# Optimization experiments

Measured on AMD Instinct MI355X. Metric: run time of the kernel, lower is better.

Reference implementation:

```python
import jax, jax.numpy as jnp
import numpy as np

N_DRUG = 10000
N_DIS = 10000
FM = 256
FD = 256
E = 320000
LAYERS = 5
OC = 128


def setup_inputs() -> dict:
    key = jax.random.key(0)
    ks = jax.random.split(key, 24)
    s = 1.0 / np.sqrt(FM)  # keep 5 stacked relu-GCN layers numerically tame
    return {
        "x_m": jax.random.normal(ks[0], (N_DRUG, FM), jnp.float32),
        "x_d": jax.random.normal(ks[1], (N_DIS, FD), jnp.float32),
        "w_m": jax.random.uniform(ks[2], (E,), jnp.float32),
        "w_d": jax.random.uniform(ks[3], (E,), jnp.float32),
        "Wx": jax.random.normal(ks[4], (LAYERS, FM, FM), jnp.float32) * s,
        "bx": jnp.zeros((LAYERS, FM), jnp.float32),
        "Wy": jax.random.normal(ks[5], (LAYERS, FD, FD), jnp.float32) * s,
        "by": jnp.zeros((LAYERS, FD), jnp.float32),
        "fc1x_w": jax.random.normal(ks[6], (5 * LAYERS, LAYERS), jnp.float32) * 0.3,
        "fc1x_b": jnp.zeros((5 * LAYERS,), jnp.float32),
        "fc2x_w": jax.random.normal(ks[7], (LAYERS, 5 * LAYERS), jnp.float32) * 0.2,
        "fc2x_b": jnp.zeros((LAYERS,), jnp.float32),
        "fc1y_w": jax.random.normal(ks[8], (5 * LAYERS, LAYERS), jnp.float32) * 0.3,
        "fc1y_b": jnp.zeros((5 * LAYERS,), jnp.float32),
        "fc2y_w": jax.random.normal(ks[9], (LAYERS, 5 * LAYERS), jnp.float32) * 0.2,
        "fc2y_b": jnp.zeros((LAYERS,), jnp.float32),
        "cnnx_w": jax.random.normal(ks[10], (OC, LAYERS, FM, 1), jnp.float32) * 0.05,
        "cnnx_b": jnp.zeros((OC,), jnp.float32),
        "cnny_w": jax.random.normal(ks[11], (OC, LAYERS, FD, 1), jnp.float32) * 0.05,
        "cnny_b": jnp.zeros((OC,), jnp.float32),
        "edges_m": jax.random.randint(ks[12], (2, E), 0, N_DRUG, jnp.int32),
        "edges_d": jax.random.randint(ks[13], (2, E), 0, N_DIS, jnp.int32),
    }


def _gcn_layer(x, W, b, src, dst, ew, n):
    """PyG GCNConv: add self-loops (weight 1), symmetric normalization,
    weighted scatter-add aggregation, then bias."""
    loops = jnp.arange(n)
    src2 = jnp.concatenate([src, loops])
    dst2 = jnp.concatenate([dst, loops])
    w2 = jnp.concatenate([ew, jnp.ones((n,), x.dtype)])
    deg = jax.ops.segment_sum(w2, dst2, num_segments=n)
    dinv = jnp.where(deg > 0, jax.lax.rsqrt(deg), 0.0)
    norm = dinv[src2] * w2 * dinv[dst2]          # [E+n]
    h = x @ W                                     # [n, f]
    agg = jax.ops.segment_sum(norm[:, None] * h[src2], dst2, num_segments=n)
    return agg + b


def _branch(x0, W, b, src, dst, ew, fc1w, fc1b, fc2w, fc2b, cw, cb):
    n = x0.shape[0]
    feats = []
    h = x0
    for i in range(LAYERS):
        h = jax.nn.relu(_gcn_layer(h, W[i], b[i], src, dst, ew, n))
        feats.append(h.T)                          # [f, n]
    X = jnp.stack(feats)                           # [C=5, f, n]  (== XM.view)
    att = jnp.max(X, axis=(1, 2))                  # global max pool -> [5]
    att = jax.nn.relu(att @ fc1w.T + fc1b)
    att = jax.nn.sigmoid(att @ fc2w.T + fc2b)      # [5]
    Xa = jax.nn.relu(att[:, None, None] * X)       # channel attention
    # conv with kernel (f,1): out[o,n] = sum_{c,f} cw[o,c,f,0] * Xa[c,f,n]
    out = jnp.einsum('ocf,cfn->on', cw[..., 0], Xa) + cb[:, None]
    return out.T                                   # [n, out_channels]


def reference(x_m, x_d, w_m, w_d, Wx, bx, Wy, by,
              fc1x_w, fc1x_b, fc2x_w, fc2x_b,
              fc1y_w, fc1y_b, fc2y_w, fc2y_b,
              cnnx_w, cnnx_b, cnny_w, cnny_b,
              edges_m, edges_d):
    x = _branch(x_m, Wx, bx, edges_m[0], edges_m[1], w_m,
                fc1x_w, fc1x_b, fc2x_w, fc2x_b, cnnx_w, cnnx_b)
    y = _branch(x_d, Wy, by, edges_d[0], edges_d[1], w_d,
                fc1y_w, fc1y_b, fc2y_w, fc2y_b, cnny_w, cnny_b)
    return x @ y.T                                 # [N_drug, N_disease]
```

## Files before the change

kernel.cpp:

```cpp
#include <hip/hip_runtime.h>
#include <hip/hip_bf16.h>
#include <math.h>

#define N_NODES 10000
#define FEAT    256
#define NEDGE   320000
#define NLAYERS 5
#define NOC     128

#define NTILE   79
#define PADROWS 10112
#define PACKSZ  1294336

typedef __attribute__((ext_vector_type(8))) short bf16x8;
typedef __attribute__((ext_vector_type(4))) float f32x4;

__global__ void k_init(float* deg, int* cnt, int* fill, int* attm) {
    int i = blockIdx.x * blockDim.x + threadIdx.x;
    if (i < N_NODES) { deg[i] = 1.0f; cnt[i] = 0; fill[i] = 0; }
    if (i < NLAYERS) attm[i] = 0;
}

__global__ void k_count(const int* __restrict__ edges, const float* __restrict__ ew,
                        float* deg, int* cnt) {
    int e = blockIdx.x * blockDim.x + threadIdx.x;
    if (e >= NEDGE) return;
    int d = edges[NEDGE + e];
    atomicAdd(&deg[d], ew[e]);
    atomicAdd(&cnt[d], 1);
}

__global__ void k_dinv(float* deg) {
    int i = blockIdx.x * blockDim.x + threadIdx.x;
    if (i < N_NODES) {
        float dg = deg[i];
        deg[i] = (dg > 0.f) ? 1.0f / sqrtf(dg) : 0.f;
    }
}

__global__ void k_scan(const int* __restrict__ cnt, int* __restrict__ ptr) {
    __shared__ int sm[1024];
    __shared__ int carry;
    int t = threadIdx.x;
    if (t == 0) carry = 0;
    __syncthreads();
    for (int base = 0; base < N_NODES; base += 1024) {
        int i = base + t;
        int v = (i < N_NODES) ? cnt[i] : 0;
        sm[t] = v;
        __syncthreads();
        for (int off = 1; off < 1024; off <<= 1) {
            int add = (t >= off) ? sm[t - off] : 0;
            __syncthreads();
            sm[t] += add;
            __syncthreads();
        }
        if (i < N_NODES) ptr[i] = carry + sm[t] - v;
        __syncthreads();
        if (t == 1023) carry += sm[1023];
        __syncthreads();
    }
    if (t == 0) ptr[N_NODES] = carry;
}

__global__ void k_fill(const int* __restrict__ edges, const float* __restrict__ ew,
                       const float* __restrict__ dinv, const int* __restrict__ ptr,
                       int* fill, int* __restrict__ col, float* __restrict__ val) {
    int e = blockIdx.x * blockDim.x + threadIdx.x;
    if (e >= NEDGE) return;
    int s = edges[e], d = edges[NEDGE + e];
    int pos = ptr[d] + atomicAdd(&fill[d], 1);
    col[pos] = s;
    val[pos] = dinv[s] * ew[e] * dinv[d];
}

__global__ __launch_bounds__(256) void k_spmm(const float* __restrict__ x,
        const int* __restrict__ ptr, const int* __restrict__ col,
        const float* __restrict__ val, const float* __restrict__ dinv,
        float* __restrict__ t) {
    int wave = threadIdx.x >> 6;
    int lane = threadIdx.x & 63;
    int row = blockIdx.x * 4 + wave;
    if (row >= N_NODES) return;
    float di = dinv[row];
    float selfc = di * di;
    float4 xv = ((const float4*)(x + (size_t)row * FEAT))[lane];
    float4 acc;
    acc.x = selfc * xv.x; acc.y = selfc * xv.y; acc.z = selfc * xv.z; acc.w = selfc * xv.w;
    int e0 = ptr[row], e1 = ptr[row + 1];
    for (int e = e0; e < e1; ++e) {
        int c = col[e];
        float cv = val[e];
        float4 v = ((const float4*)(x + (size_t)c * FEAT))[lane];
        acc.x += cv * v.x; acc.y += cv * v.y; acc.z += cv * v.z; acc.w += cv * v.w;
    }
    ((float4*)(t + (size_t)row * FEAT))[lane] = acc;
}

__global__ __launch_bounds__(256) void k_gemm(const float* __restrict__ A,
        const float* __restrict__ B, const float* __restrict__ bias,
        float* __restrict__ C, int M, int N, int K, int chunked,
        int* attm, int do_relu) {
    __shared__ float As[16][68];
    __shared__ float Bs[16][68];
    int tid = threadIdx.x;
    int tx = tid & 15, ty = tid >> 4;
    int m0 = blockIdx.x * 64, n0 = blockIdx.y * 64;
    float acc[4][4];
#pragma unroll
    for (int i = 0; i < 4; ++i)
#pragma unroll
        for (int j = 0; j < 4; ++j) acc[i][j] = 0.f;

    int arow = m0 + (tid >> 2); if (arow >= M) arow = M - 1;
    int am = tid >> 2;
    int akk = (tid & 3) * 4;
    int bk = tid >> 4;
    int bn = (tid & 15) * 4;

    for (int k0 = 0; k0 < K; k0 += 16) {
        int ka = k0 + akk;
        float4 av;
        if (chunked)
            av = *(const float4*)(A + ((size_t)(ka >> 8) * N_NODES + arow) * FEAT + (ka & 255));
        else
            av = *(const float4*)(A + (size_t)arow * K + ka);
        float4 bv = *(const float4*)(B + (size_t)(k0 + bk) * N + (n0 + bn));
        __syncthreads();
        As[akk + 0][am] = av.x;
        As[akk + 1][am] = av.y;
        As[akk + 2][am] = av.z;
        As[akk + 3][am] = av.w;
        *(float4*)&Bs[bk][bn] = bv;
        __syncthreads();
#pragma unroll
        for (int kk = 0; kk < 16; ++kk) {
            float4 a4 = *(const float4*)&As[kk][ty * 4];
            float4 b4 = *(const float4*)&Bs[kk][tx * 4];
            float a[4] = {a4.x, a4.y, a4.z, a4.w};
            float b[4] = {b4.x, b4.y, b4.z, b4.w};
#pragma unroll
            for (int i = 0; i < 4; ++i)
#pragma unroll
                for (int j = 0; j < 4; ++j) acc[i][j] += a[i] * b[j];
        }
    }

    float lmax = 0.f;
#pragma unroll
    for (int i = 0; i < 4; ++i) {
        int m = m0 + ty * 4 + i;
        if (m < M) {
            float vals[4];
#pragma unroll
            for (int j = 0; j < 4; ++j) {
                float v = acc[i][j] + bias[n0 + tx * 4 + j];
                if (do_relu) { v = fmaxf(v, 0.f); lmax = fmaxf(lmax, v); }
                vals[j] = v;
            }
            *(float4*)(C + (size_t)m * N + n0 + tx * 4) =
                make_float4(vals[0], vals[1], vals[2], vals[3]);
        }
    }
    if (do_relu) {
        __syncthreads();
        float* red = (float*)As;
        red[tid] = lmax;
        __syncthreads();
        for (int s = 128; s > 0; s >>= 1) {
            if (tid < s) red[tid] = fmaxf(red[tid], red[tid + s]);
            __syncthreads();
        }
        if (tid == 0) atomicMax(attm, __float_as_int(red[0]));
    }
}

__global__ void k_att(const int* __restrict__ attm, const float* __restrict__ fc1w,
                      const float* __restrict__ fc1b, const float* __restrict__ fc2w,
                      const float* __restrict__ fc2b, float* __restrict__ att) {
    __shared__ float a0[NLAYERS], a1[5 * NLAYERS];
    int t = threadIdx.x;
    if (t < NLAYERS) a0[t] = __int_as_float(attm[t]);
    __syncthreads();
    if (t < 5 * NLAYERS) {
        float s = fc1b[t];
        for (int c = 0; c < NLAYERS; ++c) s += fc1w[t * NLAYERS + c] * a0[c];
        a1[t] = fmaxf(s, 0.f);
    }
    __syncthreads();
    if (t < NLAYERS) {
        float s = fc2b[t];
        for (int c = 0; c < 5 * NLAYERS; ++c) s += fc2w[t * 5 * NLAYERS + c] * a1[c];
        att[t] = 1.f / (1.f + expf(-s));
    }
}

__global__ void k_bprime(const float* __restrict__ cw, const float* __restrict__ att,
                         float* __restrict__ bp) {
    int idx = blockIdx.x * blockDim.x + threadIdx.x;
    if (idx >= NLAYERS * FEAT * NOC) return;
    int k = idx >> 7;
    int o = idx & (NOC - 1);
    bp[idx] = cw[(size_t)o * (NLAYERS * FEAT) + k] * att[k >> 8];
}

__global__ __launch_bounds__(256) void k_pack(const float* __restrict__ src,
        ushort* __restrict__ hi, ushort* __restrict__ lo) {
    int t = blockIdx.x * blockDim.x + threadIdx.x;
    int row = t >> 4;
    int g = t & 15;
    int mt = row >> 4, rr = row & 15;
    int ks = g >> 2, kg = g & 3;
    size_t dst = ((size_t)(mt * 4 + ks) * 64 + kg * 16 + rr) * 8;
    uint h[4] = {0, 0, 0, 0}, l[4] = {0, 0, 0, 0};
    if (row < N_NODES) {
        const float* p = src + (size_t)row * NOC + g * 8;
#pragma unroll
        for (int e = 0; e < 8; ++e) {
            float x = p[e];
            __hip_bfloat16 hb = __float2bfloat16(x);
            float hf = __bfloat162float(hb);
            __hip_bfloat16 lb = __float2bfloat16(x - hf);
            uint hu = *(const ushort*)&hb;
            uint lu = *(const ushort*)&lb;
            h[e >> 1] |= hu << ((e & 1) * 16);
            l[e >> 1] |= lu << ((e & 1) * 16);
        }
    }
    *(uint4*)(hi + dst) = make_uint4(h[0], h[1], h[2], h[3]);
    *(uint4*)(lo + dst) = make_uint4(l[0], l[1], l[2], l[3]);
}

__global__ __launch_bounds__(256) void k_final_mfma(
        const ushort* __restrict__ xh, const ushort* __restrict__ xl,
        const ushort* __restrict__ yh, const ushort* __restrict__ yl,
        float* __restrict__ C) {
    int bid = blockIdx.x;
    const int nwg = NTILE * NTILE;
    const int q = nwg >> 3, r = nwg & 7;
    int xcd = bid & 7, loc = bid >> 3;
    int wg = (xcd < r ? xcd * (q + 1) : r * (q + 1) + (xcd - r) * q) + loc;
    int tm = wg / NTILE, tn = wg % NTILE;

    int tid = threadIdx.x;
    int wave = tid >> 6, lane = tid & 63;
    int m0 = tm * 128 + (wave >> 1) * 64;
    int n0 = tn * 128 + (wave & 1) * 64;
    int mtb = m0 >> 4, ntb = n0 >> 4;

    f32x4 acc[4][4];
#pragma unroll
    for (int i = 0; i < 4; ++i)
#pragma unroll
        for (int j = 0; j < 4; ++j) acc[i][j] = (f32x4){0.f, 0.f, 0.f, 0.f};

#pragma unroll
    for (int ks = 0; ks < 4; ++ks) {
        bf16x8 ah[4], al[4], bh[4], bl[4];
#pragma unroll
        for (int i = 0; i < 4; ++i) {
            size_t ao = ((size_t)((mtb + i) * 4 + ks) * 64 + lane) * 8;
            size_t bo = ((size_t)((ntb + i) * 4 + ks) * 64 + lane) * 8;
            ah[i] = *(const bf16x8*)(xh + ao);
            al[i] = *(const bf16x8*)(xl + ao);
            bh[i] = *(const bf16x8*)(yh + bo);
            bl[i] = *(const bf16x8*)(yl + bo);
        }
#pragma unroll
        for (int i = 0; i < 4; ++i)
#pragma unroll
            for (int j = 0; j < 4; ++j) {
                acc[i][j] = __builtin_amdgcn_mfma_f32_16x16x32_bf16(ah[i], bh[j], acc[i][j], 0, 0, 0);
                acc[i][j] = __builtin_amdgcn_mfma_f32_16x16x32_bf16(ah[i], bl[j], acc[i][j], 0, 0, 0);
                acc[i][j] = __builtin_amdgcn_mfma_f32_16x16x32_bf16(al[i], bh[j], acc[i][j], 0, 0, 0);
            }
    }

    int rbase = (lane >> 4) * 4, cn = lane & 15;
    bool full = (m0 + 63 < N_NODES) && (n0 + 63 < N_NODES);
    if (full) {
#pragma unroll
        for (int i = 0; i < 4; ++i)
#pragma unroll
            for (int j = 0; j < 4; ++j) {
                size_t base = (size_t)(m0 + i * 16 + rbase) * N_NODES + (n0 + j * 16 + cn);
#pragma unroll
                for (int rr = 0; rr < 4; ++rr)
                    C[base + (size_t)rr * N_NODES] = acc[i][j][rr];
            }
    } else {
        for (int i = 0; i < 4; ++i)
            for (int j = 0; j < 4; ++j) {
                int ccol = n0 + j * 16 + cn;
                if (ccol >= N_NODES) continue;
                for (int rr = 0; rr < 4; ++rr) {
                    int mr = m0 + i * 16 + rbase + rr;
                    if (mr < N_NODES)
                        C[(size_t)mr * N_NODES + ccol] = acc[i][j][rr];
                }
            }
    }
}

extern "C" void kernel_launch(void* const* d_in, const int* in_sizes, int n_in,
                              void* d_out, int out_size, void* d_ws, size_t ws_size,
                              hipStream_t stream) {
    (void)in_sizes; (void)n_in; (void)out_size; (void)ws_size;

    float* ws     = (float*)d_ws;
    float* feats  = ws;
    float* tbuf   = feats + 12800000;
    float* outx   = tbuf + 2560000;
    float* outy   = outx + 1280000;
    float* dinv   = outy + 1280000;
    float* val    = dinv + 10016;
    float* bprime = val + 320000;
    float* attF   = bprime + 163840;
    int*   ptr    = (int*)(attF + 16);
    int*   cnt    = ptr + 10016;
    int*   fill   = cnt + 10016;
    int*   col    = fill + 10016;
    int*   attm   = col + 320000;

    ushort* pxh = (ushort*)feats;
    ushort* pxl = pxh + PACKSZ;
    ushort* pyh = pxl + PACKSZ;
    ushort* pyl = pyh + PACKSZ;

    for (int b = 0; b < 2; ++b) {
        const float* x0   = (const float*)d_in[b == 0 ? 0 : 1];
        const float* ew   = (const float*)d_in[b == 0 ? 2 : 3];
        const float* W    = (const float*)d_in[b == 0 ? 4 : 6];
        const float* bias = (const float*)d_in[b == 0 ? 5 : 7];
        const float* fc1w = (const float*)d_in[b == 0 ? 8 : 12];
        const float* fc1b = (const float*)d_in[b == 0 ? 9 : 13];
        const float* fc2w = (const float*)d_in[b == 0 ? 10 : 14];
        const float* fc2b = (const float*)d_in[b == 0 ? 11 : 15];
        const float* cw   = (const float*)d_in[b == 0 ? 16 : 18];
        const float* cb   = (const float*)d_in[b == 0 ? 17 : 19];
        const int* edges  = (const int*)d_in[b == 0 ? 20 : 21];
        float* outb = (b == 0) ? outx : outy;

        k_init<<<40, 256, 0, stream>>>(dinv, cnt, fill, attm);
        k_count<<<1250, 256, 0, stream>>>(edges, ew, dinv, cnt);
        k_dinv<<<40, 256, 0, stream>>>(dinv);
        k_scan<<<1, 1024, 0, stream>>>(cnt, ptr);
        k_fill<<<1250, 256, 0, stream>>>(edges, ew, dinv, ptr, fill, col, val);

        for (int l = 0; l < NLAYERS; ++l) {
            const float* prev = (l == 0) ? x0 : (feats + (size_t)(l - 1) * N_NODES * FEAT);
            k_spmm<<<2500, 256, 0, stream>>>(prev, ptr, col, val, dinv, tbuf);
            k_gemm<<<dim3(157, 4), 256, 0, stream>>>(
                tbuf, W + (size_t)l * FEAT * FEAT, bias + (size_t)l * FEAT,
                feats + (size_t)l * N_NODES * FEAT,
                N_NODES, FEAT, FEAT, 0, attm + l, 1);
        }

        k_att<<<1, 64, 0, stream>>>(attm, fc1w, fc1b, fc2w, fc2b, attF);
        k_bprime<<<640, 256, 0, stream>>>(cw, attF, bprime);
        k_gemm<<<dim3(157, 2), 256, 0, stream>>>(
            feats, bprime, cb, outb, N_NODES, NOC, NLAYERS * FEAT, 1, nullptr, 0);
    }

    k_pack<<<632, 256, 0, stream>>>(outx, pxh, pxl);
    k_pack<<<632, 256, 0, stream>>>(outy, pyh, pyl);
    k_final_mfma<<<NTILE * NTILE, 256, 0, stream>>>(pxh, pxl, pyh, pyl, (float*)d_out);
}
```

Before: 1.661 ms.

## Move per-layer GCN GEMM to split-fp16 MFMA with packed operands

The SpMM now writes its output directly as packed fp16 hi/lo pairs in MFMA fragment layout. A new kernel packs the weights the same way, and a new MFMA GEMM kernel replaces the fp32 SIMT tiled GEMM for the per-layer transform. That kernel fuses bias, ReLU and the global-max reduction for attention. The final GEMM also switches from bf16 to fp16 splitting, which gives more mantissa precision but less exponent range. The goal is to cut the FMA-bound fp32 GEMM time, at the cost of three MFMAs per tile and the risk of fp16 overflow or underflow.

Result: faster. 1.603 ms (-3.5%).

```diff
diff --git a/kernel.cpp b/kernel.cpp
--- a/kernel.cpp
+++ b/kernel.cpp
@@ -12,8 +12,17 @@
 #define PADROWS 10112
 #define PACKSZ  1294336
 
-typedef __attribute__((ext_vector_type(8))) short bf16x8;
+typedef __attribute__((ext_vector_type(8))) _Float16 f16x8;
 typedef __attribute__((ext_vector_type(4))) float f32x4;
+
+static __device__ inline void f16split(float x, ushort& h, ushort& l) {
+    _Float16 hf = (_Float16)x;
+    float hb = (float)hf;
+    _Float16 lf = (_Float16)(x - hb);
+    union { _Float16 f; ushort u; } ch, cl;
+    ch.f = hf; cl.f = lf;
+    h = ch.u; l = cl.u;
+}
 
 __global__ void k_init(float* deg, int* cnt, int* fill, int* attm) {
     int i = blockIdx.x * blockDim.x + threadIdx.x;
@@ -77,7 +86,7 @@
 __global__ __launch_bounds__(256) void k_spmm(const float* __restrict__ x,
         const int* __restrict__ ptr, const int* __restrict__ col,
         const float* __restrict__ val, const float* __restrict__ dinv,
-        float* __restrict__ t) {
+        ushort* __restrict__ th, ushort* __restrict__ tl) {
     int wave = threadIdx.x >> 6;
     int lane = threadIdx.x & 63;
     int row = blockIdx.x * 4 + wave;
@@ -94,7 +103,105 @@
         float4 v = ((const float4*)(x + (size_t)c * FEAT))[lane];
         acc.x += cv * v.x; acc.y += cv * v.y; acc.z += cv * v.z; acc.w += cv * v.w;
     }
-    ((float4*)(t + (size_t)row * FEAT))[lane] = acc;
+    int mt = row >> 4, rr = row & 15;
+    int ks = lane >> 3, kg = (lane >> 1) & 3, ee = (lane & 1) * 4;
+    size_t pb = ((size_t)(mt * 8 + ks) * 64 + kg * 16 + rr) * 8 + ee;
+    ushort h[4], l[4];
+    f16split(acc.x, h[0], l[0]); f16split(acc.y, h[1], l[1]);
+    f16split(acc.z, h[2], l[2]); f16split(acc.w, h[3], l[3]);
+    *(uint2*)(th + pb) = make_uint2((uint)h[0] | ((uint)h[1] << 16),
+                                    (uint)h[2] | ((uint)h[3] << 16));
+    *(uint2*)(tl + pb) = make_uint2((uint)l[0] | ((uint)l[1] << 16),
+                                    (uint)l[2] | ((uint)l[3] << 16));
+}
+
+__global__ void k_packW(const float* __restrict__ W, ushort* __restrict__ wh,
+                        ushort* __restrict__ wl) {
+    int g = blockIdx.x * blockDim.x + threadIdx.x;
+    if (g >= NLAYERS * 8192) return;
+    int l = g >> 13, gl = g & 8191;
+    int rc = gl & 15, kg = (gl >> 4) & 3, ks = (gl >> 6) & 7, nt = gl >> 9;
+    int n = nt * 16 + rc, k0 = ks * 32 + kg * 8;
+    const float* src = W + (size_t)l * 65536 + (size_t)k0 * 256 + n;
+    uint hw[4], lw[4];
+#pragma unroll
+    for (int e = 0; e < 8; e += 2) {
+        ushort h0, l0, h1, l1;
+        f16split(src[(size_t)e * 256], h0, l0);
+        f16split(src[(size_t)(e + 1) * 256], h1, l1);
+        hw[e >> 1] = (uint)h0 | ((uint)h1 << 16);
+        lw[e >> 1] = (uint)l0 | ((uint)l1 << 16);
+    }
+    size_t dst = (size_t)g * 8;
+    *(uint4*)(wh + dst) = make_uint4(hw[0], hw[1], hw[2], hw[3]);
+    *(uint4*)(wl + dst) = make_uint4(lw[0], lw[1], lw[2], lw[3]);
+}
+
+__global__ __launch_bounds__(256) void k_gemm_l(
+        const ushort* __restrict__ th, const ushort* __restrict__ tl,
+        const ushort* __restrict__ wh, const ushort* __restrict__ wl,
+        const float* __restrict__ bias, float* __restrict__ out, int* attm) {
+    __shared__ float red[256];
+    int tid = threadIdx.x;
+    int wave = tid >> 6, lane = tid & 63;
+    int m0 = blockIdx.x * 128 + (wave >> 1) * 64;
+    int n0 = blockIdx.y * 128 + (wave & 1) * 64;
+    int mtb = m0 >> 4, ntb = n0 >> 4;
+
+    f32x4 acc[4][4];
+#pragma unroll
+    for (int i = 0; i < 4; ++i)
+#pragma unroll
+        for (int j = 0; j < 4; ++j) acc[i][j] = (f32x4){0.f, 0.f, 0.f, 0.f};
+
+#pragma unroll
+    for (int ks = 0; ks < 8; ++ks) {
+        f16x8 ah[4], al[4], bh[4], bl[4];
+#pragma unroll
+        for (int i = 0; i < 4; ++i) {
+            int mt = mtb + i; if (mt > 624) mt = 624;
+            size_t ao = ((size_t)(mt * 8 + ks) * 64 + lane) * 8;
+            size_t bo = ((size_t)((ntb + i) * 8 + ks) * 64 + lane) * 8;
+            ah[i] = *(const f16x8*)(th + ao);
+            al[i] = *(const f16x8*)(tl + ao);
+            bh[i] = *(const f16x8*)(wh + bo);
+            bl[i] = *(const f16x8*)(wl + bo);
+        }
+#pragma unroll
+        for (int i = 0; i < 4; ++i)
+#pragma unroll
+            for (int j = 0; j < 4; ++j) {
+                acc[i][j] = __builtin_amdgcn_mfma_f32_16x16x32_f16(ah[i], bh[j], acc[i][j], 0, 0, 0);
+                acc[i][j] = __builtin_amdgcn_mfma_f32_16x16x32_f16(ah[i], bl[j], acc[i][j], 0, 0, 0);
+                acc[i][j] = __builtin_amdgcn_mfma_f32_16x16x32_f16(al[i], bh[j], acc[i][j], 0, 0, 0);
+            }
+    }
+
+    int rbase = (lane >> 4) * 4, cn = lane & 15;
+    float lmax = 0.f;
+#pragma unroll
+    for (int i = 0; i < 4; ++i)
+#pragma unroll
+        for (int j = 0; j < 4; ++j) {
+            int n = n0 + j * 16 + cn;
+            float bv = bias[n];
+#pragma unroll
+            for (int rr = 0; rr < 4; ++rr) {
+                int m = m0 + i * 16 + rbase + rr;
+                if (m < N_NODES) {
+                    float v = fmaxf(acc[i][j][rr] + bv, 0.f);
+                    lmax = fmaxf(lmax, v);
+                    out[(size_t)m * FEAT + n] = v;
+                }
+            }
+        }
+    red[tid] = lmax;
+    __syncthreads();
+    for (int s = 128; s > 0; s >>= 1) {
+        if (tid < s) red[tid] = fmaxf(red[tid], red[tid + s]);
+        __syncthreads();
+    }
+    if (tid == 0) atomicMax(attm, __float_as_int(red[0]));
 }
 
 __global__ __launch_bounds__(256) void k_gemm(const float* __restrict__ A,
@@ -217,14 +324,10 @@
         const float* p = src + (size_t)row * NOC + g * 8;
 #pragma unroll
         for (int e = 0; e < 8; ++e) {
-            float x = p[e];
-            __hip_bfloat16 hb = __float2bfloat16(x);
-            float hf = __bfloat162float(hb);
-            __hip_bfloat16 lb = __float2bfloat16(x - hf);
-            uint hu = *(const ushort*)&hb;
-            uint lu = *(const ushort*)&lb;
-            h[e >> 1] |= hu << ((e & 1) * 16);
-            l[e >> 1] |= lu << ((e & 1) * 16);
+            ushort hu, lu;
+            f16split(p[e], hu, lu);
+            h[e >> 1] |= (uint)hu << ((e & 1) * 16);
+            l[e >> 1] |= (uint)lu << ((e & 1) * 16);
         }
     }
     *(uint4*)(hi + dst) = make_uint4(h[0], h[1], h[2], h[3]);
@@ -256,23 +359,23 @@
 
 #pragma unroll
     for (int ks = 0; ks < 4; ++ks) {
-        bf16x8 ah[4], al[4], bh[4], bl[4];
+        f16x8 ah[4], al[4], bh[4], bl[4];
 #pragma unroll
         for (int i = 0; i < 4; ++i) {
             size_t ao = ((size_t)((mtb + i) * 4 + ks) * 64 + lane) * 8;
             size_t bo = ((size_t)((ntb + i) * 4 + ks) * 64 + lane) * 8;
-            ah[i] = *(const bf16x8*)(xh + ao);
-            al[i] = *(const bf16x8*)(xl + ao);
-            bh[i] = *(const bf16x8*)(yh + bo);
-            bl[i] = *(const bf16x8*)(yl + bo);
+            ah[i] = *(const f16x8*)(xh + ao);
+            al[i] = *(const f16x8*)(xl + ao);
+            bh[i] = *(const f16x8*)(yh + bo);
+            bl[i] = *(const f16x8*)(yl + bo);
         }
 #pragma unroll
         for (int i = 0; i < 4; ++i)
 #pragma unroll
             for (int j = 0; j < 4; ++j) {
-                acc[i][j] = __builtin_amdgcn_mfma_f32_16x16x32_bf16(ah[i], bh[j], acc[i][j], 0, 0, 0);
-                acc[i][j] = __builtin_amdgcn_mfma_f32_16x16x32_bf16(ah[i], bl[j], acc[i][j], 0, 0, 0);
-                acc[i][j] = __builtin_amdgcn_mfma_f32_16x16x32_bf16(al[i], bh[j], acc[i][j], 0, 0, 0);
+                acc[i][j] = __builtin_amdgcn_mfma_f32_16x16x32_f16(ah[i], bh[j], acc[i][j], 0, 0, 0);
+                acc[i][j] = __builtin_amdgcn_mfma_f32_16x16x32_f16(ah[i], bl[j], acc[i][j], 0, 0, 0);
+                acc[i][j] = __builtin_amdgcn_mfma_f32_16x16x32_f16(al[i], bh[j], acc[i][j], 0, 0, 0);
             }
     }
 
@@ -322,6 +425,11 @@
     int*   col    = fill + 10016;
     int*   attm   = col + 320000;
 
+    ushort* th = (ushort*)tbuf;
+    ushort* tl = th + 2560000;
+    ushort* Wh = (ushort*)outy;
+    ushort* Wl = Wh + NLAYERS * 65536;
+
     ushort* pxh = (ushort*)feats;
     ushort* pxl = pxh + PACKSZ;
     ushort* pyh = pxl + PACKSZ;
@@ -346,14 +454,15 @@
         k_dinv<<<40, 256, 0, stream>>>(dinv);
         k_scan<<<1, 1024, 0, stream>>>(cnt, ptr);
         k_fill<<<1250, 256, 0, stream>>>(edges, ew, dinv, ptr, fill, col, val);
+        k_packW<<<160, 256, 0, stream>>>(W, Wh, Wl);
 
         for (int l = 0; l < NLAYERS; ++l) {
             const float* prev = (l == 0) ? x0 : (feats + (size_t)(l - 1) * N_NODES * FEAT);
-            k_spmm<<<2500, 256, 0, stream>>>(prev, ptr, col, val, dinv, tbuf);
-            k_gemm<<<dim3(157, 4), 256, 0, stream>>>(
-                tbuf, W + (size_t)l * FEAT * FEAT, bias + (size_t)l * FEAT,
-                feats + (size_t)l * N_NODES * FEAT,
-                N_NODES, FEAT, FEAT, 0, attm + l, 1);
+            k_spmm<<<2500, 256, 0, stream>>>(prev, ptr, col, val, dinv, th, tl);
+            k_gemm_l<<<dim3(79, 2), 256, 0, stream>>>(
+                th, tl, Wh + (size_t)l * 65536, Wl + (size_t)l * 65536,
+                bias + (size_t)l * FEAT,
+                feats + (size_t)l * N_NODES * FEAT, attm + l);
         }
 
         k_att<<<1, 64, 0, stream>>>(attm, fc1w, fc1b, fc2w, fc2b, attF);
```
